# Optimization experiments

Hardware: AMD Instinct MI355X
Metric: run time of the kernel (lower is better)

## Reference

```python
import jax, jax.numpy as jnp
import numpy as np

B, T, M, F, H, O = 64, 168, 256, 32, 128, 32
TWO_OVER_PI = 2.0 / np.pi


def setup_inputs() -> dict:
    key = jax.random.key(0)
    ks = jax.random.split(key, 8)
    return {
        "x": jax.random.normal(ks[0], (B, T, M, F), dtype=jnp.float32),
        "assoc_W": jax.random.normal(ks[1], (F, M, M), dtype=jnp.float32) * (1.0 / np.sqrt(M)),
        "W_ih": jax.random.normal(ks[2], (4 * H, F), dtype=jnp.float32) * (1.0 / np.sqrt(F)),
        "W_hh": jax.random.normal(ks[3], (4 * H, H), dtype=jnp.float32) * (1.0 / np.sqrt(H)),
        "b_ih": jax.random.normal(ks[4], (4 * H,), dtype=jnp.float32) * 0.01,
        "b_hh": jax.random.normal(ks[5], (4 * H,), dtype=jnp.float32) * 0.01,
        "dense_W": jax.random.normal(ks[6], (O, H), dtype=jnp.float32) * (1.0 / np.sqrt(H)),
        "dense_b": jax.random.normal(ks[7], (O,), dtype=jnp.float32) * 0.01,
    }


def _forward(x, assoc_W, W_ih, W_hh, b_ih, b_hh, dense_W, dense_b):
    # x: [B, T, M, F] (batch_first) -> scan over time
    xt = jnp.transpose(x, (1, 0, 2, 3))  # [T, B, M, F]
    b, m = x.shape[0], x.shape[2]
    h0 = jnp.zeros((b, m, H), dtype=x.dtype)
    c0 = jnp.zeros((b, m, H), dtype=x.dtype)

    def step(carry, xin):
        h, c = carry
        # ArcTanNorm: squash into (-1, 1)
        y = jnp.arctan(xin) * TWO_OVER_PI                      # [B, M, F]
        # ICFA: per-attribute association across map units
        y = jnp.einsum('amn,bna->bma', assoc_W, y)             # [B, M, F]
        # LSTM cell (shared weights across map units), PyTorch gate order i,f,g,o
        gates = (jnp.einsum('bmf,gf->bmg', y, W_ih) + b_ih
                 + jnp.einsum('bmh,gh->bmg', h, W_hh) + b_hh)  # [B, M, 4H]
        i, f, g, o = jnp.split(gates, 4, axis=-1)
        i, f, o = jax.nn.sigmoid(i), jax.nn.sigmoid(f), jax.nn.sigmoid(o)
        g = jnp.tanh(g)
        c = f * c + i * g
        h = o * jnp.tanh(c)
        # Dense output head
        out = jnp.einsum('bmh,oh->bmo', h, dense_W) + dense_b  # [B, M, O]
        return (h, c), out

    _, outs = jax.lax.scan(step, (h0, c0), xt)                 # [T, B, M, O]
    return jnp.transpose(outs, (1, 0, 2, 3))                   # [B, T, M, O]


def reference(x, assoc_W, W_ih, W_hh, b_ih, b_hh, dense_W, dense_b):
    return _forward(x, assoc_W, W_ih, W_hh, b_ih, b_hh, dense_W, dense_b)
```

## Files before the change

### kernel.cpp

```cpp
#include <hip/hip_runtime.h>

#define B_  64
#define T_  168
#define M_  256
#define F_  32
#define H_  128
#define O_  32
#define BT_ (B_*T_)

typedef __attribute__((ext_vector_type(8))) short bh8;
typedef __attribute__((ext_vector_type(4))) short sh4;
typedef __attribute__((ext_vector_type(4))) float fx4;
typedef __attribute__((ext_vector_type(2))) float fx2;

static __device__ __forceinline__ short f2bf(float f) {
  unsigned u = __float_as_uint(f);
  u += 0x7FFFu + ((u >> 16) & 1u);
  return (short)(u >> 16);
}
static __device__ __forceinline__ float ex2_(float x) {
#if __has_builtin(__builtin_amdgcn_exp2f)
  return __builtin_amdgcn_exp2f(x);
#else
  return exp2f(x);
#endif
}
static __device__ __forceinline__ float rcp_(float x) {
#if __has_builtin(__builtin_amdgcn_rcpf)
  return __builtin_amdgcn_rcpf(x);
#else
  return 1.0f / x;
#endif
}
static __device__ __forceinline__ float sigm(float x) {
  return 1.0f / (1.0f + __expf(-x));
}
static __device__ __forceinline__ float tanh_f(float x) {
  return 1.0f - 2.0f / (1.0f + __expf(2.0f * x));
}
static __device__ __forceinline__ fx4 mm16(bh8 a, bh8 b, fx4 c) {
  return __builtin_amdgcn_mfma_f32_16x16x32_bf16(a, b, c, 0, 0, 0);
}
static __device__ __forceinline__ bh8 cvt8(fx4 p0, fx4 p1) {
  bh8 s;
  s[0] = f2bf(p0[0]); s[1] = f2bf(p0[1]); s[2] = f2bf(p0[2]); s[3] = f2bf(p0[3]);
  s[4] = f2bf(p1[0]); s[5] = f2bf(p1[1]); s[6] = f2bf(p1[2]); s[7] = f2bf(p1[3]);
  return s;
}


__global__ __launch_bounds__(512) void atan_tr(const float* __restrict__ x,
                                               short* __restrict__ ut) {
  __shared__ __align__(16) short tl[8 * 32 * 68];
  const int tid = threadIdx.x;
  const float c2p = 0.63661977236758134f;
  for (int it = 0; it < 21; ++it) {
    const int id = blockIdx.x + it * 256;
    const int bt0 = (id >> 2) * 8, n0 = (id & 3) * 64;
    if (it) __syncthreads();
#pragma unroll
    for (int i = 0; i < 8; ++i) {
      int idx = tid + i * 512;
      int aq = idx & 7, nl = (idx >> 3) & 63, btl = idx >> 9;
      const float* src = x + (long)(bt0 + btl) * 8192 + (n0 + nl) * 32 + aq * 4;
      fx4 v = *(const fx4*)src;
      int base = (btl * 32 + aq * 4) * 68 + nl;
#pragma unroll
      for (int k = 0; k < 4; ++k)
        tl[base + k * 68] = f2bf(atanf(v[k]) * c2p);
    }
    __syncthreads();
#pragma unroll
    for (int p = 0; p < 8; ++p) {
      int r = p * 32 + (tid >> 4);
      int a = r >> 3, btl = r & 7, nq = tid & 15;
      sh4 v = *(const sh4*)&tl[(btl * 32 + a) * 68 + nq * 4];
      *(sh4*)&ut[((long)a * BT_ + bt0 + btl) * 256 + n0 + nq * 4] = v;
    }
  }
}

__global__ __launch_bounds__(512) void icfa_gemm(const short* __restrict__ ut,
                                                 const float* __restrict__ aw,
                                                 short* __restrict__ y) {
  __shared__ __align__(16) short waf[8 * 8 * 64 * 8];
  __shared__ __align__(16) short ubf[64 * 256];
  const int tid = threadIdx.x;
  const int lane = tid & 63, w = tid >> 6, l15 = lane & 15, l4 = lane >> 4;
  const int a = blockIdx.x >> 3, s = blockIdx.x & 7;
  const long ua = (long)a * BT_;

  for (int mh = 0; mh < 2; ++mh) {
    __syncthreads();
    for (int i = 0; i < 8; ++i) {
      int idx = tid + i * 512;
      int ln = idx & 63, ks = (idx >> 6) & 7, mt = idx >> 9;
      const float* src = aw + a * 65536 + (mh * 128 + mt * 16 + (ln & 15)) * 256
                         + ks * 32 + (ln >> 4) * 8;
      *(bh8*)&waf[idx * 8] = cvt8(*(const fx4*)src, *(const fx4*)(src + 4));
    }
    __syncthreads();
    bh8 Af[8];
#pragma unroll
    for (int ks = 0; ks < 8; ++ks)
      Af[ks] = *(const bh8*)&waf[((w * 8 + ks) * 64 + lane) * 8];

    for (int tile = 0; tile < 21; ++tile) {
      const int bt0 = s * 1344 + tile * 64;
      __syncthreads();
#pragma unroll
      for (int i = 0; i < 4; ++i) {
        int idx = tid + i * 512;
        int row = idx >> 5, slot = idx & 31;
        bh8 v = *(const bh8*)&ut[(ua + bt0 + row) * 256 + slot * 8];
        int sb = (row * 512 + slot * 16) ^ ((row & 7) << 4);
        *(bh8*)&((char*)ubf)[sb] = v;
      }
      __syncthreads();
#pragma unroll
      for (int ct = 0; ct < 4; ++ct) {
        fx4 acc = {0.f, 0.f, 0.f, 0.f};
        const int btr = ct * 16 + l15;
#pragma unroll
        for (int ks = 0; ks < 8; ++ks) {
          int byo = (btr * 512 + ks * 64 + l4 * 16) ^ ((btr & 7) << 4);
          bh8 Bf = *(const bh8*)&((char*)ubf)[byo];
          acc = mm16(Af[ks], Bf, acc);
        }
        sh4 o;
        o[0] = f2bf(acc[0]); o[1] = f2bf(acc[1]);
        o[2] = f2bf(acc[2]); o[3] = f2bf(acc[3]);
        *(sh4*)&y[(ua + bt0 + btr) * 256 + mh * 128 + w * 16 + l4 * 4] = o;
      }
    }
  }
}

__global__ __launch_bounds__(1024, 4) void lstm_fused3(
    const short* __restrict__ y,
    const float* __restrict__ Wih, const float* __restrict__ Whh,
    const float* __restrict__ bih, const float* __restrict__ bhh,
    const float* __restrict__ dW,  const float* __restrict__ db,
    float* __restrict__ out) {
  __shared__ short whf[32 * 4 * 64 * 8];
  __shared__ short hbuf[4 * 4 * 64 * 8];
  __shared__ short ytr[4 * 64 * 8];
  __shared__ float obuf[64 * 36];
  const int tid = threadIdx.x;
  const int lane = tid & 63, w = tid >> 6, l15 = lane & 15, l4 = lane >> 4;
  const int wg = w & 7, hw = w >> 3;
  const int bidx = blockIdx.x >> 2, m0 = (blockIdx.x & 3) * 64;
  const float L2E = 1.4426950408889634f;

  for (int i = 0; i < 8; ++i) {
    int idx = tid + i * 1024;
    int ln = idx & 63, ks = (idx >> 6) & 3, ct = idx >> 8;
    const float* src = Whh + (ct * 16 + (ln & 15)) * 128 + ks * 32 + (ln >> 4) * 8;
    *(bh8*)&whf[idx * 8] = cvt8(*(const fx4*)src, *(const fx4*)(src + 4));
  }
  for (int i = 0; i < 4; ++i) ((int*)hbuf)[tid + i * 1024] = 0;

  bh8 wfih[4]; float nb[4];
#pragma unroll
  for (int gate = 0; gate < 4; ++gate) {
    int g = (gate * 8 + wg) * 16 + l15;
    float b = bih[g] + bhh[g];
    nb[gate] = (gate == 2) ? (2.0f * L2E * b) : (-L2E * b);
    const float* src = Wih + g * 32 + l4 * 8;
    wfih[gate] = cvt8(*(const fx4*)src, *(const fx4*)(src + 4));
  }
  bh8 df[4];
  const int rtd = (w >> 1) & 3, oc = w & 1;
  const int od = oc * 16 + l15;
  const float dbias = db[od];
#pragma unroll
  for (int ks = 0; ks < 4; ++ks) {
    const float* src = dW + od * 128 + ks * 32 + l4 * 8;
    df[ks] = cvt8(*(const fx4*)src, *(const fx4*)(src + 4));
  }

  float cst[2][4];
#pragma unroll
  for (int rr = 0; rr < 2; ++rr)
#pragma unroll
    for (int r = 0; r < 4; ++r) cst[rr][r] = 0.f;

  const int ar = tid >> 5, mq2 = tid & 31;
  const long yrow = (long)ar * BT_ + (long)bidx * T_;
  const int mls = tid >> 4, a0s = (tid & 15) * 2;
  const long tb0 = (long)bidx * T_ * 8192;
  const long ooff = (long)(m0 + mls) * 32 + a0s;
  const int kse = wg >> 1;
  const int lnhi = (((wg & 1) * 2 + (l15 >> 3)) << 4);
  const int e0 = l15 & 7;
  const int rt0 = hw * 2, rt1 = hw * 2 + 1;

  int ys = *(const int*)&y[(yrow + 0) * 256 + m0 + mq2 * 2];
  {
    int ml0 = mq2 * 2, ml1 = ml0 + 1;
    ytr[((ml0 >> 4) * 64 + ((ar >> 3) << 4) + (ml0 & 15)) * 8 + (ar & 7)] =
        (short)(ys & 0xffff);
    ytr[((ml1 >> 4) * 64 + ((ar >> 3) << 4) + (ml1 & 15)) * 8 + (ar & 7)] =
        (short)(((unsigned)ys) >> 16);
  }
  ys = *(const int*)&y[(yrow + 1) * 256 + m0 + mq2 * 2];
  __syncthreads();

  for (int t = 0; t < T_; ++t) {
    fx4 acc[2][4];
    {
      bh8 ya0 = *(const bh8*)&ytr[(rt0 * 64 + lane) * 8];
      bh8 ya1 = *(const bh8*)&ytr[(rt1 * 64 + lane) * 8];
      fx4 Z = {0.f, 0.f, 0.f, 0.f};
#pragma unroll
      for (int gate = 0; gate < 4; ++gate) {
        acc[0][gate] = mm16(ya0, wfih[gate], Z);
        acc[1][gate] = mm16(ya1, wfih[gate], Z);
      }
    }
#pragma unroll
    for (int ks = 0; ks < 4; ++ks) {
      bh8 hA0 = *(const bh8*)&hbuf[((rt0 * 4 + ks) * 64 + lane) * 8];
      bh8 hA1 = *(const bh8*)&hbuf[((rt1 * 4 + ks) * 64 + lane) * 8];
#pragma unroll
      for (int gate = 0; gate < 4; ++gate) {
        bh8 Bf = *(const bh8*)&whf[(((gate * 8 + wg) * 4 + ks) * 64 + lane) * 8];
        acc[0][gate] = mm16(hA0, Bf, acc[0][gate]);
        acc[1][gate] = mm16(hA1, Bf, acc[1][gate]);
      }
    }
    float hn[2][4];
#pragma unroll
    for (int rr = 0; rr < 2; ++rr)
#pragma unroll
      for (int r = 0; r < 4; ++r) {
        float iv = rcp_(1.f + ex2_(fmaf(acc[0][rr ? 1 : 0][r] * 0.f + acc[0][0][r] * 0.f
                                        + acc[rr][0][r], -L2E, nb[0])));
        iv = rcp_(1.f + ex2_(fmaf(acc[rr][0][r], -L2E, nb[0])));
        float fv = rcp_(1.f + ex2_(fmaf(acc[rr][1][r], -L2E, nb[1])));
        float ov = rcp_(1.f + ex2_(fmaf(acc[rr][3][r], -L2E, nb[3])));
        float gv = 1.f - 2.f * rcp_(1.f + ex2_(fmaf(acc[rr][2][r], 2.f * L2E, nb[2])));
        float cn = fv * cst[rr][r] + iv * gv;
        cst[rr][r] = cn;
        float th = 1.f - 2.f * rcp_(1.f + ex2_(cn * (2.f * L2E)));
        hn[rr][r] = ov * th;
      }
    __syncthreads();
#pragma unroll
    for (int rr = 0; rr < 2; ++rr)
#pragma unroll
      for (int r = 0; r < 4; ++r)
        hbuf[(((hw * 2 + rr) * 4 + kse) * 64 + lnhi + l4 * 4 + r) * 8 + e0] =
            f2bf(hn[rr][r]);
    if (t + 1 < T_) {
      int ml0 = mq2 * 2, ml1 = ml0 + 1;
      ytr[((ml0 >> 4) * 64 + ((ar >> 3) << 4) + (ml0 & 15)) * 8 + (ar & 7)] =
          (short)(ys & 0xffff);
      ytr[((ml1 >> 4) * 64 + ((ar >> 3) << 4) + (ml1 & 15)) * 8 + (ar & 7)] =
          (short)(((unsigned)ys) >> 16);
    }
    if (t + 2 < T_) ys = *(const int*)&y[(yrow + t + 2) * 256 + m0 + mq2 * 2];
    if (t > 0) {
      fx2 o2 = *(const fx2*)&obuf[mls * 36 + a0s];
      *(fx2*)&out[tb0 + (long)(t - 1) * 8192 + ooff] = o2;
    }
    __syncthreads();
    if (w < 8) {
      fx4 A = {dbias, dbias, dbias, dbias};
#pragma unroll
      for (int ks = 0; ks < 4; ++ks) {
        bh8 hA2 = *(const bh8*)&hbuf[((rtd * 4 + ks) * 64 + lane) * 8];
        A = mm16(hA2, df[ks], A);
      }
#pragma unroll
      for (int r = 0; r < 4; ++r)
        obuf[(rtd * 16 + l4 * 4 + r) * 36 + oc * 16 + l15] = A[r];
    }
  }
  __syncthreads();
  {
    fx2 o2 = *(const fx2*)&obuf[mls * 36 + a0s];
    *(fx2*)&out[tb0 + (long)(T_ - 1) * 8192 + ooff] = o2;
  }
}


__global__ __launch_bounds__(512) void icfa_mfma(const float* __restrict__ x,
                                                 const float* __restrict__ aw,
                                                 float* __restrict__ y) {
  __shared__ short waf[8 * 8 * 64 * 8];
  __shared__ short ubf[64 * 264];
  const int tid = threadIdx.x;
  const int lane = tid & 63, w = tid >> 6, l15 = lane & 15, l4 = lane >> 4;
  const int a = blockIdx.x >> 3, s = blockIdx.x & 7;
  const float c2p = 0.63661977236758134f;

  for (int mh = 0; mh < 2; ++mh) {
    __syncthreads();
    for (int i = 0; i < 8; ++i) {
      int idx = tid + i * 512;
      int ln = idx & 63, ks = (idx >> 6) & 7, mt = idx >> 9;
      const float* src = aw + a * 65536 + (mh * 128 + mt * 16 + (ln & 15)) * 256
                         + ks * 32 + (ln >> 4) * 8;
      *(bh8*)&waf[idx * 8] = cvt8(*(const fx4*)src, *(const fx4*)(src + 4));
    }
    __syncthreads();
    bh8 Af[8];
#pragma unroll
    for (int ks = 0; ks < 8; ++ks)
      Af[ks] = *(const bh8*)&waf[((w * 8 + ks) * 64 + lane) * 8];

    for (int tile = 0; tile < 21; ++tile) {
      const int bt0 = s * 1344 + tile * 64;
      __syncthreads();
#pragma unroll 4
      for (int i = 0; i < 32; ++i) {
        int idx = tid + i * 512;
        int n = idx & 255, btc = idx >> 8;
        float v = x[(long)(bt0 + btc) * 8192 + n * 32 + a];
        ubf[btc * 264 + n] = f2bf(atanf(v) * c2p);
      }
      __syncthreads();
#pragma unroll
      for (int ct = 0; ct < 4; ++ct) {
        fx4 acc = {0.f, 0.f, 0.f, 0.f};
#pragma unroll
        for (int ks = 0; ks < 8; ++ks) {
          bh8 Bf = *(const bh8*)&ubf[(ct * 16 + l15) * 264 + ks * 32 + l4 * 8];
          acc = mm16(Af[ks], Bf, acc);
        }
        long ybase = (long)(bt0 + ct * 16 + l15) * 8192
                     + (mh * 128 + w * 16 + l4 * 4) * 32 + a;
#pragma unroll
        for (int r = 0; r < 4; ++r) y[ybase + (long)r * 32] = acc[r];
      }
    }
  }
}

__global__ __launch_bounds__(512) void lstm_fused(
    const float* __restrict__ Wih, const float* __restrict__ Whh,
    const float* __restrict__ bih, const float* __restrict__ bhh,
    const float* __restrict__ dW,  const float* __restrict__ db,
    float* __restrict__ yo) {
  __shared__ short whf[32 * 4 * 64 * 8];
  __shared__ short hbuf[4 * 4 * 64 * 8];
  __shared__ short ytr[4 * 64 * 8];
  __shared__ float obuf[64 * 36];
  const int tid = threadIdx.x;
  const int lane = tid & 63, w = tid >> 6, l15 = lane & 15, l4 = lane >> 4;
  const int bidx = blockIdx.x >> 2, m0 = (blockIdx.x & 3) * 64;

  for (int i = 0; i < 16; ++i) {
    int idx = tid + i * 512;
    int ln = idx & 63, ks = (idx >> 6) & 3, ct = idx >> 8;
    const float* src = Whh + (ct * 16 + (ln & 15)) * 128 + ks * 32 + (ln >> 4) * 8;
    *(bh8*)&whf[idx * 8] = cvt8(*(const fx4*)src, *(const fx4*)(src + 4));
  }
  for (int i = 0; i < 8; ++i) ((int*)hbuf)[tid + i * 512] = 0;

  bh8 wfih[4]; float bias[4];
#pragma unroll
  for (int gate = 0; gate < 4; ++gate) {
    int g = (gate * 8 + w) * 16 + l15;
    bias[gate] = bih[g] + bhh[g];
    const float* src = Wih + g * 32 + l4 * 8;
    wfih[gate] = cvt8(*(const fx4*)src, *(const fx4*)(src + 4));
  }
  bh8 df[4];
  const int rtd = w >> 1, oc = w & 1;
  const int od = oc * 16 + l15;
  const float dbias = db[od];
#pragma unroll
  for (int ks = 0; ks < 4; ++ks) {
    const float* src = dW + od * 128 + ks * 32 + l4 * 8;
    df[ks] = cvt8(*(const fx4*)src, *(const fx4*)(src + 4));
  }

  float cst[4][4];
#pragma unroll
  for (int rt = 0; rt < 4; ++rt)
#pragma unroll
    for (int r = 0; r < 4; ++r) cst[rt][r] = 0.f;

  const int mloc = tid >> 3, a0 = (tid & 7) * 4;
  const long tb0 = (long)bidx * T_ * 8192;
  const long pfoff = (long)(m0 + mloc) * 32 + a0;
  const int ytre = ((mloc >> 4) * 64 + ((a0 >> 3) << 4) + (mloc & 15)) * 8 + (a0 & 7);
  const int kse = w >> 1;
  const int lnhi = (((w & 1) * 2 + (l15 >> 3)) << 4);
  const int e0 = l15 & 7;

  fx4 y4 = *(const fx4*)&yo[tb0 + pfoff];
  {
    sh4 p; p[0] = f2bf(y4[0]); p[1] = f2bf(y4[1]); p[2] = f2bf(y4[2]); p[3] = f2bf(y4[3]);
    *(sh4*)&ytr[ytre] = p;
  }
  y4 = *(const fx4*)&yo[tb0 + 8192 + pfoff];
  __syncthreads();

  for (int t = 0; t < T_; ++t) {
    const long off = tb0 + (long)t * 8192;
    float hn[4][4];
    bh8 Ball[4][4];
#pragma unroll
    for (int gate = 0; gate < 4; ++gate)
#pragma unroll
      for (int ks = 0; ks < 4; ++ks)
        Ball[gate][ks] =
            *(const bh8*)&whf[((((gate * 8 + w) * 4) + ks) * 64 + lane) * 8];
#pragma unroll
    for (int rt = 0; rt < 4; ++rt) {
      bh8 ya = *(const bh8*)&ytr[(rt * 64 + lane) * 8];
      bh8 hA[4];
#pragma unroll
      for (int ks = 0; ks < 4; ++ks)
        hA[ks] = *(const bh8*)&hbuf[((rt * 4 + ks) * 64 + lane) * 8];
      fx4 acc[4];
#pragma unroll
      for (int gate = 0; gate < 4; ++gate) {
        fx4 A = {bias[gate], bias[gate], bias[gate], bias[gate]};
        A = mm16(ya, wfih[gate], A);
#pragma unroll
        for (int ks = 0; ks < 4; ++ks) A = mm16(hA[ks], Ball[gate][ks], A);
        acc[gate] = A;
      }
#pragma unroll
      for (int r = 0; r < 4; ++r) {
        float iv = sigm(acc[0][r]);
        float fv = sigm(acc[1][r]);
        float gv = tanh_f(acc[2][r]);
        float ov = sigm(acc[3][r]);
        float cn = fv * cst[rt][r] + iv * gv;
        cst[rt][r] = cn;
        hn[rt][r] = ov * tanh_f(cn);
      }
    }
    __syncthreads();
#pragma unroll
    for (int rt = 0; rt < 4; ++rt)
#pragma unroll
      for (int r = 0; r < 4; ++r)
        hbuf[((rt * 4 + kse) * 64 + lnhi + l4 * 4 + r) * 8 + e0] = f2bf(hn[rt][r]);
    if (t + 1 < T_) {
      sh4 p; p[0] = f2bf(y4[0]); p[1] = f2bf(y4[1]); p[2] = f2bf(y4[2]); p[3] = f2bf(y4[3]);
      *(sh4*)&ytr[ytre] = p;
    }
    if (t + 2 < T_) y4 = *(const fx4*)&yo[off + 2 * 8192 + pfoff];
    __syncthreads();
    {
      fx4 A = {dbias, dbias, dbias, dbias};
#pragma unroll
      for (int ks = 0; ks < 4; ++ks) {
        bh8 hA2 = *(const bh8*)&hbuf[((rtd * 4 + ks) * 64 + lane) * 8];
        A = mm16(hA2, df[ks], A);
      }
#pragma unroll
      for (int r = 0; r < 4; ++r)
        obuf[(rtd * 16 + l4 * 4 + r) * 36 + oc * 16 + l15] = A[r];
    }
    __syncthreads();
    {
      fx4 o4 = *(const fx4*)&obuf[mloc * 36 + a0];
      *(fx4*)&yo[off + pfoff] = o4;
    }
  }
}

extern "C" void kernel_launch(void* const* d_in, const int* in_sizes, int n_in,
                              void* d_out, int out_size, void* d_ws, size_t ws_size,
                              hipStream_t stream) {
  const float* x   = (const float*)d_in[0];
  const float* aw  = (const float*)d_in[1];
  const float* wih = (const float*)d_in[2];
  const float* whh = (const float*)d_in[3];
  const float* bih = (const float*)d_in[4];
  const float* bhh = (const float*)d_in[5];
  const float* dw  = (const float*)d_in[6];
  const float* db  = (const float*)d_in[7];
  float* out = (float*)d_out;

  const size_t PLANE = (size_t)32 * BT_ * 256;
  const size_t NEED  = 2 * PLANE * sizeof(short);
  if (d_ws && ws_size >= NEED) {
    short* u = (short*)d_ws;
    short* y = u + PLANE;
    hipLaunchKernelGGL(atan_tr,   dim3(256), dim3(512), 0, stream, x, u);
    hipLaunchKernelGGL(icfa_gemm, dim3(256), dim3(512), 0, stream, u, aw, y);
    hipLaunchKernelGGL(lstm_fused3, dim3(256), dim3(1024), 0, stream,
                       y, wih, whh, bih, bhh, dw, db, out);
  } else {
    hipLaunchKernelGGL(icfa_mfma, dim3(256), dim3(512), 0, stream, x, aw, out);
    hipLaunchKernelGGL(lstm_fused, dim3(256), dim3(512), 0, stream,
                       wih, whh, bih, bhh, dw, db, out);
  }
}
```

Before: 912.0 us.

## Fold dense head into next LSTM step, drop second barrier, swizzle h layout

The LSTM kernel now computes the dense output head for step t-1 at the start of step t, reading the previous hidden state before the barrier. Each step therefore needs one __syncthreads instead of two, and the obuf staging plus its coalesced copy-out go away; outputs are written directly to global memory. The Whh fragments are reordered so each wave walks a contiguous per-wave region, and the h buffer gets an XOR-swizzled layout with packed bf16 conversion via v_cvt_pk_bf16_f32. The prefetch of y moves to the top of the loop. Dense results are now stored as strided scalar writes, which are less coalesced than before.

New measurement: 856.2 us. -6.1%, faster.

```diff
diff --git a/kernel.cpp b/kernel.cpp
--- a/kernel.cpp
+++ b/kernel.cpp
@@ -11,12 +11,16 @@
 typedef __attribute__((ext_vector_type(8))) short bh8;
 typedef __attribute__((ext_vector_type(4))) short sh4;
 typedef __attribute__((ext_vector_type(4))) float fx4;
-typedef __attribute__((ext_vector_type(2))) float fx2;
 
 static __device__ __forceinline__ short f2bf(float f) {
   unsigned u = __float_as_uint(f);
   u += 0x7FFFu + ((u >> 16) & 1u);
   return (short)(u >> 16);
+}
+static __device__ __forceinline__ unsigned cvtpk(float lo, float hi) {
+  unsigned r;
+  asm("v_cvt_pk_bf16_f32 %0, %1, %2" : "=v"(r) : "v"(lo), "v"(hi));
+  return r;
 }
 static __device__ __forceinline__ float ex2_(float x) {
 #if __has_builtin(__builtin_amdgcn_exp2f)
@@ -136,16 +140,15 @@
   }
 }
 
-__global__ __launch_bounds__(1024, 4) void lstm_fused3(
+__global__ __launch_bounds__(1024) void lstm_fused4(
     const short* __restrict__ y,
     const float* __restrict__ Wih, const float* __restrict__ Whh,
     const float* __restrict__ bih, const float* __restrict__ bhh,
     const float* __restrict__ dW,  const float* __restrict__ db,
     float* __restrict__ out) {
-  __shared__ short whf[32 * 4 * 64 * 8];
-  __shared__ short hbuf[4 * 4 * 64 * 8];
-  __shared__ short ytr[4 * 64 * 8];
-  __shared__ float obuf[64 * 36];
+  __shared__ __align__(16) short whf[65536];
+  __shared__ __align__(16) short hx[8192];
+  __shared__ __align__(16) short ytr[2048];
   const int tid = threadIdx.x;
   const int lane = tid & 63, w = tid >> 6, l15 = lane & 15, l4 = lane >> 4;
   const int wg = w & 7, hw = w >> 3;
@@ -154,11 +157,12 @@
 
   for (int i = 0; i < 8; ++i) {
     int idx = tid + i * 1024;
-    int ln = idx & 63, ks = (idx >> 6) & 3, ct = idx >> 8;
-    const float* src = Whh + (ct * 16 + (ln & 15)) * 128 + ks * 32 + (ln >> 4) * 8;
+    int ln = idx & 63, ks = (idx >> 6) & 3, gate = (idx >> 8) & 3, wgp = idx >> 10;
+    const float* src = Whh + ((gate * 8 + wgp) * 16 + (ln & 15)) * 128
+                       + ks * 32 + (ln >> 4) * 8;
     *(bh8*)&whf[idx * 8] = cvt8(*(const fx4*)src, *(const fx4*)(src + 4));
   }
-  for (int i = 0; i < 4; ++i) ((int*)hbuf)[tid + i * 1024] = 0;
+  for (int i = 0; i < 4; ++i) ((int*)hx)[tid + i * 1024] = 0;
 
   bh8 wfih[4]; float nb[4];
 #pragma unroll
@@ -170,7 +174,7 @@
     wfih[gate] = cvt8(*(const fx4*)src, *(const fx4*)(src + 4));
   }
   bh8 df[4];
-  const int rtd = (w >> 1) & 3, oc = w & 1;
+  const int rt_d = 2 * hw + (wg & 1), oc = (wg >> 1) & 1;
   const int od = oc * 16 + l15;
   const float dbias = db[od];
 #pragma unroll
@@ -185,15 +189,16 @@
 #pragma unroll
     for (int r = 0; r < 4; ++r) cst[rr][r] = 0.f;
 
+  const char* hxc = (const char*)hx;
+  const int rbase = (hw * 32 + l15) * 64 + ((l4 * 16) ^ ((l15 >> 2) << 4));
+  const int wbase = (wg >> 1) * 4096 + (hw * 32 + l4 * 4) * 64
+                  + ((2 * ((wg & 1) * 16 + l15)) ^ (l4 << 4));
+  const int dbase = rbase + (wg & 1) * 1024;
+  const int wfb = wg * 16384 + lane * 16;
   const int ar = tid >> 5, mq2 = tid & 31;
   const long yrow = (long)ar * BT_ + (long)bidx * T_;
-  const int mls = tid >> 4, a0s = (tid & 15) * 2;
-  const long tb0 = (long)bidx * T_ * 8192;
-  const long ooff = (long)(m0 + mls) * 32 + a0s;
-  const int kse = wg >> 1;
-  const int lnhi = (((wg & 1) * 2 + (l15 >> 3)) << 4);
-  const int e0 = l15 & 7;
-  const int rt0 = hw * 2, rt1 = hw * 2 + 1;
+  const long obB = (long)bidx * T_ * 8192
+                 + (long)(m0 + rt_d * 16 + l4 * 4) * 32 + od;
 
   int ys = *(const int*)&y[(yrow + 0) * 256 + m0 + mq2 * 2];
   {
@@ -207,36 +212,47 @@
   __syncthreads();
 
   for (int t = 0; t < T_; ++t) {
+    int ysn = 0;
+    if (t + 2 < T_) ysn = *(const int*)&y[(yrow + t + 2) * 256 + m0 + mq2 * 2];
     fx4 acc[2][4];
     {
-      bh8 ya0 = *(const bh8*)&ytr[(rt0 * 64 + lane) * 8];
-      bh8 ya1 = *(const bh8*)&ytr[(rt1 * 64 + lane) * 8];
+      bh8 ya0 = *(const bh8*)&ytr[((2 * hw) * 64 + lane) * 8];
+      bh8 ya1 = *(const bh8*)&ytr[((2 * hw + 1) * 64 + lane) * 8];
       fx4 Z = {0.f, 0.f, 0.f, 0.f};
 #pragma unroll
-      for (int gate = 0; gate < 4; ++gate) {
-        acc[0][gate] = mm16(ya0, wfih[gate], Z);
-        acc[1][gate] = mm16(ya1, wfih[gate], Z);
+      for (int g = 0; g < 4; ++g) {
+        acc[0][g] = mm16(ya0, wfih[g], Z);
+        acc[1][g] = mm16(ya1, wfih[g], Z);
       }
     }
 #pragma unroll
     for (int ks = 0; ks < 4; ++ks) {
-      bh8 hA0 = *(const bh8*)&hbuf[((rt0 * 4 + ks) * 64 + lane) * 8];
-      bh8 hA1 = *(const bh8*)&hbuf[((rt1 * 4 + ks) * 64 + lane) * 8];
-#pragma unroll
-      for (int gate = 0; gate < 4; ++gate) {
-        bh8 Bf = *(const bh8*)&whf[(((gate * 8 + wg) * 4 + ks) * 64 + lane) * 8];
-        acc[0][gate] = mm16(hA0, Bf, acc[0][gate]);
-        acc[1][gate] = mm16(hA1, Bf, acc[1][gate]);
-      }
+      bh8 h0 = *(const bh8*)(hxc + rbase + ks * 4096);
+      bh8 h1 = *(const bh8*)(hxc + rbase + 1024 + ks * 4096);
+#pragma unroll
+      for (int g = 0; g < 4; ++g) {
+        bh8 Bf = *(const bh8*)((const char*)whf + wfb + (g * 4 + ks) * 1024);
+        acc[0][g] = mm16(h0, Bf, acc[0][g]);
+        acc[1][g] = mm16(h1, Bf, acc[1][g]);
+      }
+    }
+    if (wg < 4 && t > 0) {
+      fx4 A = {dbias, dbias, dbias, dbias};
+#pragma unroll
+      for (int ks = 0; ks < 4; ++ks) {
+        bh8 hd = *(const bh8*)(hxc + dbase + ks * 4096);
+        A = mm16(hd, df[ks], A);
+      }
+      float* op = out + obB + (long)(t - 1) * 8192;
+#pragma unroll
+      for (int ri = 0; ri < 4; ++ri) op[ri * 32] = A[ri];
     }
     float hn[2][4];
 #pragma unroll
     for (int rr = 0; rr < 2; ++rr)
 #pragma unroll
       for (int r = 0; r < 4; ++r) {
-        float iv = rcp_(1.f + ex2_(fmaf(acc[0][rr ? 1 : 0][r] * 0.f + acc[0][0][r] * 0.f
-                                        + acc[rr][0][r], -L2E, nb[0])));
-        iv = rcp_(1.f + ex2_(fmaf(acc[rr][0][r], -L2E, nb[0])));
+        float iv = rcp_(1.f + ex2_(fmaf(acc[rr][0][r], -L2E, nb[0])));
         float fv = rcp_(1.f + ex2_(fmaf(acc[rr][1][r], -L2E, nb[1])));
         float ov = rcp_(1.f + ex2_(fmaf(acc[rr][3][r], -L2E, nb[3])));
         float gv = 1.f - 2.f * rcp_(1.f + ex2_(fmaf(acc[rr][2][r], 2.f * L2E, nb[2])));
@@ -247,11 +263,15 @@
       }
     __syncthreads();
 #pragma unroll
-    for (int rr = 0; rr < 2; ++rr)
-#pragma unroll
-      for (int r = 0; r < 4; ++r)
-        hbuf[(((hw * 2 + rr) * 4 + kse) * 64 + lnhi + l4 * 4 + r) * 8 + e0] =
-            f2bf(hn[rr][r]);
+    for (int rr = 0; rr < 2; ++rr) {
+      unsigned p01 = cvtpk(hn[rr][0], hn[rr][1]);
+      unsigned p23 = cvtpk(hn[rr][2], hn[rr][3]);
+      short* bp = (short*)((char*)hx + wbase + rr * 1024);
+      bp[0]  = (short)(p01 & 0xffff);
+      bp[32] = (short)(p01 >> 16);
+      bp[64] = (short)(p23 & 0xffff);
+      bp[96] = (short)(p23 >> 16);
+    }
     if (t + 1 < T_) {
       int ml0 = mq2 * 2, ml1 = ml0 + 1;
       ytr[((ml0 >> 4) * 64 + ((ar >> 3) << 4) + (ml0 & 15)) * 8 + (ar & 7)] =
@@ -259,28 +279,19 @@
       ytr[((ml1 >> 4) * 64 + ((ar >> 3) << 4) + (ml1 & 15)) * 8 + (ar & 7)] =
           (short)(((unsigned)ys) >> 16);
     }
-    if (t + 2 < T_) ys = *(const int*)&y[(yrow + t + 2) * 256 + m0 + mq2 * 2];
-    if (t > 0) {
-      fx2 o2 = *(const fx2*)&obuf[mls * 36 + a0s];
-      *(fx2*)&out[tb0 + (long)(t - 1) * 8192 + ooff] = o2;
-    }
-    __syncthreads();
-    if (w < 8) {
-      fx4 A = {dbias, dbias, dbias, dbias};
-#pragma unroll
-      for (int ks = 0; ks < 4; ++ks) {
-        bh8 hA2 = *(const bh8*)&hbuf[((rtd * 4 + ks) * 64 + lane) * 8];
-        A = mm16(hA2, df[ks], A);
-      }
-#pragma unroll
-      for (int r = 0; r < 4; ++r)
-        obuf[(rtd * 16 + l4 * 4 + r) * 36 + oc * 16 + l15] = A[r];
-    }
-  }
-  __syncthreads();
-  {
-    fx2 o2 = *(const fx2*)&obuf[mls * 36 + a0s];
-    *(fx2*)&out[tb0 + (long)(T_ - 1) * 8192 + ooff] = o2;
+    ys = ysn;
+    __syncthreads();
+  }
+  if (wg < 4) {
+    fx4 A = {dbias, dbias, dbias, dbias};
+#pragma unroll
+    for (int ks = 0; ks < 4; ++ks) {
+      bh8 hd = *(const bh8*)(hxc + dbase + ks * 4096);
+      A = mm16(hd, df[ks], A);
+    }
+    float* op = out + obB + (long)(T_ - 1) * 8192;
+#pragma unroll
+    for (int ri = 0; ri < 4; ++ri) op[ri * 32] = A[ri];
   }
 }
 
@@ -484,11 +495,11 @@
   const size_t NEED  = 2 * PLANE * sizeof(short);
   if (d_ws && ws_size >= NEED) {
     short* u = (short*)d_ws;
-    short* y = u + PLANE;
+    short* yv = u + PLANE;
     hipLaunchKernelGGL(atan_tr,   dim3(256), dim3(512), 0, stream, x, u);
-    hipLaunchKernelGGL(icfa_gemm, dim3(256), dim3(512), 0, stream, u, aw, y);
-    hipLaunchKernelGGL(lstm_fused3, dim3(256), dim3(1024), 0, stream,
-                       y, wih, whh, bih, bhh, dw, db, out);
+    hipLaunchKernelGGL(icfa_gemm, dim3(256), dim3(512), 0, stream, u, aw, yv);
+    hipLaunchKernelGGL(lstm_fused4, dim3(256), dim3(1024), 0, stream,
+                       yv, wih, whh, bih, bhh, dw, db, out);
   } else {
     hipLaunchKernelGGL(icfa_mfma, dim3(256), dim3(512), 0, stream, x, aw, out);
     hipLaunchKernelGGL(lstm_fused, dim3(256), dim3(512), 0, stream,
```
